# Performance work log

Hardware: AMD Instinct MI355X
Metric: run time of the kernel (lower is better)

## Reference

```python
import jax, jax.numpy as jnp
import numpy as np

NUM_HEADS = 16

def setup_inputs() -> dict:
    key = jax.random.key(0)
    ks = jax.random.split(key, 5)
    d_model = 1024
    x = jax.random.normal(ks[0], (2, 2048, d_model), dtype=jnp.float32)
    # xavier-uniform-like scale for square [d_model, d_model] weights
    lim = float(np.sqrt(6.0 / (d_model + d_model)))
    def w(k):
        return jax.random.uniform(k, (d_model, d_model), dtype=jnp.float32, minval=-lim, maxval=lim)
    return {"x": x, "Wq": w(ks[1]), "Wk": w(ks[2]), "Wv": w(ks[3]), "Wo": w(ks[4])}

def reference(x, Wq, Wk, Wv, Wo):
    B, S, D = x.shape
    H = NUM_HEADS
    dk = D // H
    # project: torch does x @ W.T
    def split_heads(t):
        return t.reshape(B, S, H, dk).transpose(0, 2, 1, 3)  # [B,H,S,dk]
    q = split_heads(x @ Wq.T)
    k = split_heads(x @ Wk.T)
    v = split_heads(x @ Wv.T)
    scores = jnp.einsum('bhqd,bhkd->bhqk', q, k) / jnp.sqrt(jnp.float32(dk))
    causal = jnp.tril(jnp.ones((S, S), dtype=bool))  # True where attended
    scores = jnp.where(causal[None, None], scores, -jnp.inf)
    probs = jax.nn.softmax(scores, axis=-1)
    out = jnp.einsum('bhqk,bhkd->bhqd', probs, v)  # [B,H,S,dk]
    out = out.transpose(0, 2, 1, 3).reshape(B, S, D)
    return out @ Wo.T
```

## Files before the change

### kernel.cpp

```cpp
#include <hip/hip_runtime.h>
#include <stdint.h>

#define BATCH  2
#define SEQ    2048
#define DMODEL 1024
#define NHEADS 16
#define DKH    64
#define MTOT   (BATCH*SEQ)
#define VSTR   (SEQ + 32)

typedef unsigned short u16;
typedef __bf16 bf16x8 __attribute__((ext_vector_type(8)));
typedef float  f32x4  __attribute__((ext_vector_type(4)));

extern "C" __device__ float __ocml_native_exp2_f32(float);

__device__ __forceinline__ u16 f2bf(float f) {
  union { float f; uint32_t u; } v; v.f = f;
  uint32_t u = v.u;
  return (u16)((u + 0x7FFFu + ((u >> 16) & 1u)) >> 16);
}
__device__ __forceinline__ float bf2f(u16 h) {
  union { uint32_t u; float f; } v; v.u = (uint32_t)h << 16; return v.f;
}

__device__ __forceinline__ void gld_lds16(const void* g, void* l) {
  __builtin_amdgcn_global_load_lds(
      (__attribute__((address_space(1))) void*)g,
      (__attribute__((address_space(3))) void*)l, 16, 0, 0);
}

__device__ __forceinline__ uint32_t cvtpk(float lo, float hi) {
  uint32_t r;
  asm("v_cvt_pk_bf16_f32 %0, %1, %2" : "=v"(r) : "v"(lo), "v"(hi));
  return r;
}
__device__ __forceinline__ void pl16swap(uint32_t& a, uint32_t& b) {
  asm volatile("v_permlane16_swap_b32 %0, %1" : "+v"(a), "+v"(b));
}

__global__ void cvt_all(const float* __restrict__ x, const float* __restrict__ wa,
                        const float* __restrict__ wb, const float* __restrict__ wc,
                        const float* __restrict__ wd,
                        u16* __restrict__ xb, u16* __restrict__ wdst) {
  const int blk = blockIdx.x;
  const int tid = threadIdx.x;
  if (blk < 4096) {
    size_t o = (size_t)blk * 1024 + tid * 4;
    float4 f = *(const float4*)(x + o);
    ushort4 p;
    p.x = f2bf(f.x); p.y = f2bf(f.y); p.z = f2bf(f.z); p.w = f2bf(f.w);
    *(ushort4*)(xb + o) = p;
  } else {
    int j = blk - 4096;
    const float* ws[4] = {wa, wb, wc, wd};
    size_t src_o = (size_t)(j & 1023) * 1024 + tid * 4;
    size_t dst_o = (size_t)j * 1024 + tid * 4;
    float4 f = *(const float4*)(ws[j >> 10] + src_o);
    ushort4 p;
    p.x = f2bf(f.x); p.y = f2bf(f.y); p.z = f2bf(f.z); p.w = f2bf(f.w);
    *(ushort4*)(wdst + dst_o) = p;
  }
}

__global__ __launch_bounds__(256, 3) void gemm_qkv(
    const u16* __restrict__ xb, const u16* __restrict__ wq,
    const u16* __restrict__ wk, const u16* __restrict__ wv,
    u16* __restrict__ q, u16* __restrict__ k, u16* __restrict__ v, float qscale) {
  __shared__ __align__(16) u16 lA[128 * 64];
  __shared__ __align__(16) u16 lB[3][64 * 64];

  const int tid  = threadIdx.x;
  const int lane = tid & 63;
  const int lrow = lane & 15;
  const int quad = lane >> 4;
  const int wave = tid >> 6;
  const int wm   = (wave & 1) * 64;
  const int wn   = (wave >> 1) * 32;
  const int sx   = lrow & 7;
  const int m0 = blockIdx.x * 128, n0 = blockIdx.y * 64;
  const u16* Ws[3] = {wq, wk, wv};

  f32x4 acc[3][4][2] = {};

  for (int k0 = 0; k0 < DMODEL; k0 += 64) {
    #pragma unroll
    for (int r = 0; r < 4; ++r) {
      int off  = r * 4096 + tid * 16;
      int row  = off >> 7;
      int c16  = (off >> 4) & 7;
      int colb = (c16 ^ (row & 7)) << 4;
      gld_lds16((const char*)xb + ((size_t)(m0 + row) * DMODEL + k0) * 2 + colb,
                (char*)lA + off);
    }
    #pragma unroll
    for (int z = 0; z < 3; ++z)
      #pragma unroll
      for (int r = 0; r < 2; ++r) {
        int off  = r * 4096 + tid * 16;
        int row  = off >> 7;
        int c16  = (off >> 4) & 7;
        int colb = (c16 ^ (row & 7)) << 4;
        gld_lds16((const char*)Ws[z] + ((size_t)(n0 + row) * DMODEL + k0) * 2 + colb,
                  (char*)&lB[z][0] + off);
      }
    __syncthreads();
    #pragma unroll
    for (int ks = 0; ks < 2; ++ks) {
      const int ro = ((((ks << 2) | quad) ^ sx) << 3);
      bf16x8 a[4], b[3][2];
      #pragma unroll
      for (int i = 0; i < 4; ++i)
        a[i] = *(const bf16x8*)(lA + (wm + i*16 + lrow) * 64 + ro);
      #pragma unroll
      for (int z = 0; z < 3; ++z)
        #pragma unroll
        for (int j = 0; j < 2; ++j)
          b[z][j] = *(const bf16x8*)(&lB[z][0] + (wn + j*16 + lrow) * 64 + ro);
      #pragma unroll
      for (int z = 0; z < 3; ++z)
        #pragma unroll
        for (int i = 0; i < 4; ++i)
          #pragma unroll
          for (int j = 0; j < 2; ++j)
            acc[z][i][j] = __builtin_amdgcn_mfma_f32_16x16x32_bf16(a[i], b[z][j], acc[z][i][j], 0, 0, 0);
    }
    __syncthreads();
  }

  const int rb = quad * 4, cb = lrow;
  const int h  = blockIdx.y;
  u16* outs[3] = {q, k, v};
  #pragma unroll
  for (int z = 0; z < 3; ++z) {
    u16* out = outs[z];
    if (z == 2) {
      #pragma unroll
      for (int i = 0; i < 4; ++i)
        #pragma unroll
        for (int j = 0; j < 2; ++j) {
          int row0 = m0 + wm + i*16 + rb;
          int d_   = wn + j*16 + cb;
          int b_ = row0 >> 11, s0 = row0 & 2047;
          ushort4 pk;
          pk.x = f2bf(acc[z][i][j][0]); pk.y = f2bf(acc[z][i][j][1]);
          pk.z = f2bf(acc[z][i][j][2]); pk.w = f2bf(acc[z][i][j][3]);
          *(ushort4*)&out[((size_t)(b_*NHEADS + h) * DKH + d_) * VSTR + s0] = pk;
        }
    } else {
      const float scale = (z == 0) ? qscale : 1.0f;
      #pragma unroll
      for (int i = 0; i < 4; ++i)
        #pragma unroll
        for (int j = 0; j < 2; ++j)
          #pragma unroll
          for (int r = 0; r < 4; ++r) {
            int row = m0 + wm + i*16 + rb + r;
            int d_  = wn + j*16 + cb;
            int b_ = row >> 11, s_ = row & 2047;
            out[(((size_t)(b_*NHEADS + h) * SEQ + s_) << 6) + d_] =
                f2bf(acc[z][i][j][r] * scale);
          }
    }
  }
}

__device__ __forceinline__ void gemm_core64(const u16* A, const u16* W,
                                            int m0, int n0, f32x4 acc[4][2],
                                            u16* lA, u16* lB) {
  const int tid  = threadIdx.x;
  const int lane = tid & 63;
  const int lrow = lane & 15;
  const int quad = lane >> 4;
  const int wave = tid >> 6;
  const int wm   = (wave & 1) * 64;
  const int wn   = (wave >> 1) * 32;
  const int sx   = lrow & 7;

  for (int k0 = 0; k0 < DMODEL; k0 += 64) {
    #pragma unroll
    for (int r = 0; r < 4; ++r) {
      int off  = r * 4096 + tid * 16;
      int row  = off >> 7;
      int c16  = (off >> 4) & 7;
      int colb = (c16 ^ (row & 7)) << 4;
      gld_lds16((const char*)A + ((size_t)(m0 + row) * DMODEL + k0) * 2 + colb,
                (char*)lA + off);
    }
    #pragma unroll
    for (int r = 0; r < 2; ++r) {
      int off  = r * 4096 + tid * 16;
      int row  = off >> 7;
      int c16  = (off >> 4) & 7;
      int colb = (c16 ^ (row & 7)) << 4;
      gld_lds16((const char*)W + ((size_t)(n0 + row) * DMODEL + k0) * 2 + colb,
                (char*)lB + off);
    }
    __syncthreads();
    #pragma unroll
    for (int ks = 0; ks < 2; ++ks) {
      bf16x8 a[4], b[2];
      const int ro = ((((ks << 2) | quad) ^ sx) << 3);
      #pragma unroll
      for (int i = 0; i < 4; ++i)
        a[i] = *(const bf16x8*)(lA + (wm + i*16 + lrow) * 64 + ro);
      #pragma unroll
      for (int j = 0; j < 2; ++j)
        b[j] = *(const bf16x8*)(lB + (wn + j*16 + lrow) * 64 + ro);
      #pragma unroll
      for (int i = 0; i < 4; ++i)
        #pragma unroll
        for (int j = 0; j < 2; ++j)
          acc[i][j] = __builtin_amdgcn_mfma_f32_16x16x32_bf16(a[i], b[j], acc[i][j], 0, 0, 0);
    }
    __syncthreads();
  }
}

__global__ __launch_bounds__(256, 3) void gemm_out(
    const u16* __restrict__ ab, const u16* __restrict__ wo, float* __restrict__ out) {
  __shared__ __align__(16) u16 lA[128 * 64];
  __shared__ __align__(16) u16 lB[64 * 64];
  const int m0 = blockIdx.x * 128, n0 = blockIdx.y * 64;
  f32x4 acc[4][2] = {};
  gemm_core64(ab, wo, m0, n0, acc, lA, lB);

  const int lane = threadIdx.x & 63;
  const int wave = threadIdx.x >> 6;
  const int wm = (wave & 1) * 64, wn = (wave >> 1) * 32;
  const int rb = (lane >> 4) * 4, cb = lane & 15;
  #pragma unroll
  for (int i = 0; i < 4; ++i)
    #pragma unroll
    for (int j = 0; j < 2; ++j)
      #pragma unroll
      for (int r = 0; r < 4; ++r)
        out[(size_t)(m0 + wm + i*16 + rb + r) * DMODEL + (n0 + wn + j*16 + cb)]
            = acc[i][j][r];
}

__device__ const uint8_t JT[40] = {
  60,61,62,63, 56,57,58, 52,53,54, 48,49,50, 44,45,46, 40,41, 36,37,
  32,33, 28,29, 24, 20, 16, 12,
  59,42,25,8, 55,38,21,4, 51,34,17,0
};

__device__ __forceinline__ void stage_kv(const u16* Kg, const u16* Vg, int t,
                                         u16* lK, u16* lV, int tid) {
  #pragma unroll
  for (int r = 0; r < 2; ++r) {
    int off  = r * 4096 + tid * 16;
    int row  = off >> 7;
    int colb = (((off >> 4) & 7) ^ (row & 7)) << 4;
    gld_lds16((const char*)Kg + ((size_t)(t*64 + row) * DKH) * 2 + colb,
              (char*)lK + off);
    gld_lds16((const char*)Vg + ((size_t)row * VSTR + t*64) * 2 + colb,
              (char*)lV + off);
  }
}

__global__ __launch_bounds__(256, 3) void attn(
    const u16* __restrict__ Q, const u16* __restrict__ K,
    const u16* __restrict__ V, u16* __restrict__ O,
    u16* __restrict__ po, float* __restrict__ pl) {
  __shared__ __align__(16) u16 lK[2][64 * 64];
  __shared__ __align__(16) u16 lV[2][64 * 64];

  const int tid  = threadIdx.x;
  const int wid  = tid >> 6;
  const int lane = tid & 63;
  const int lrow = lane & 15;
  const int quad = lane >> 4;
  const int sx   = lrow & 7;
  const int pq   = ((quad & 1) << 1) | (quad >> 1);

  const int g  = blockIdx.x >> 5;
  const int bh = blockIdx.x & 31;
  const int e  = JT[g];
  const int u  = e >> 2, c = e & 3;
  const int lo = c * 8;
  const int T  = 2*u + 2;
  const int hi = (lo + 8 < T) ? lo + 8 : T;
  const int td = 2*u + (wid >> 1);
  const int qg0 = 128*u + 32*wid;

  const u16* Qg = Q + (size_t)bh * SEQ * DKH;
  const u16* Kg = K + (size_t)bh * SEQ * DKH;
  const u16* Vg = V + (size_t)bh * DKH * VSTR;

  bf16x8 aq[2][2];
  #pragma unroll
  for (int i = 0; i < 2; ++i)
    #pragma unroll
    for (int ks = 0; ks < 2; ++ks)
      aq[i][ks] = *(const bf16x8*)(Qg + (size_t)(qg0 + 16*i + lrow) * DKH + ks*32 + quad*8);

  f32x4 o_acc[2][4] = {};
  float l_acc[2] = {};

  stage_kv(Kg, Vg, lo, &lK[0][0], &lV[0][0], tid);
  __syncthreads();
  int cur = 0;

  for (int t = lo; t < hi; ++t) {
    if (t + 1 < hi)
      stage_kv(Kg, Vg, t + 1, &lK[cur ^ 1][0], &lV[cur ^ 1][0], tid);

    if (t <= td) {
      f32x4 s_acc[2][4] = {};
      {
        bf16x8 kf[2][4];
        #pragma unroll
        for (int ks = 0; ks < 2; ++ks) {
          const int kro = ((((ks << 2) | quad) ^ sx) << 3);
          #pragma unroll
          for (int j = 0; j < 4; ++j)
            kf[ks][j] = *(const bf16x8*)(&lK[cur][0] + (j*16 + lrow) * 64 + kro);
        }
        __builtin_amdgcn_s_setprio(1);
        #pragma unroll
        for (int i = 0; i < 2; ++i)
          #pragma unroll
          for (int ks = 0; ks < 2; ++ks)
            #pragma unroll
            for (int j = 0; j < 4; ++j)
              s_acc[i][j] = __builtin_amdgcn_mfma_f32_16x16x32_bf16(kf[ks][j], aq[i][ks], s_acc[i][j], 0, 0, 0);
        __builtin_amdgcn_s_setprio(0);
      }

      bf16x8 vf[2][4];
      #pragma unroll
      for (int ks = 0; ks < 2; ++ks) {
        const int vro = ((((ks << 2) | pq) ^ sx) << 3);
        #pragma unroll
        for (int j = 0; j < 4; ++j)
          vf[ks][j] = *(const bf16x8*)(&lV[cur][0] + (j*16 + lrow) * 64 + vro);
      }

      #pragma unroll
      for (int i = 0; i < 2; ++i) {
        if (t >= td) {
          const int qrel = qg0 + 16*i + lrow - 64*t;
          #pragma unroll
          for (int j = 0; j < 4; ++j) {
            int kl = j*16 + quad*4;
            #pragma unroll
            for (int r = 0; r < 4; ++r)
              if (kl + r > qrel) s_acc[i][j][r] = -1e30f;
          }
        }

        uint32_t w[4][2];
        float ls = 0.f;
        #pragma unroll
        for (int j = 0; j < 4; ++j) {
          float p0 = __ocml_native_exp2_f32(s_acc[i][j][0]);
          float p1 = __ocml_native_exp2_f32(s_acc[i][j][1]);
          float p2 = __ocml_native_exp2_f32(s_acc[i][j][2]);
          float p3 = __ocml_native_exp2_f32(s_acc[i][j][3]);
          ls += (p0 + p1) + (p2 + p3);
          w[j][0] = cvtpk(p0, p1);
          w[j][1] = cvtpk(p2, p3);
        }
        l_acc[i] += ls;

        pl16swap(w[0][0], w[1][0]);
        pl16swap(w[0][1], w[1][1]);
        pl16swap(w[2][0], w[3][0]);
        pl16swap(w[2][1], w[3][1]);
        union { uint32_t u[4]; bf16x8 v; } g0, g1;
        g0.u[0] = w[0][0]; g0.u[1] = w[0][1]; g0.u[2] = w[1][0]; g0.u[3] = w[1][1];
        g1.u[0] = w[2][0]; g1.u[1] = w[2][1]; g1.u[2] = w[3][0]; g1.u[3] = w[3][1];

        __builtin_amdgcn_s_setprio(1);
        #pragma unroll
        for (int j = 0; j < 4; ++j)
          o_acc[i][j] = __builtin_amdgcn_mfma_f32_16x16x32_bf16(g0.v, vf[0][j], o_acc[i][j], 0, 0, 0);
        #pragma unroll
        for (int j = 0; j < 4; ++j)
          o_acc[i][j] = __builtin_amdgcn_mfma_f32_16x16x32_bf16(g1.v, vf[1][j], o_acc[i][j], 0, 0, 0);
        __builtin_amdgcn_s_setprio(0);
      }
    }

    __syncthreads();
    cur ^= 1;
  }

  float lr[2][4];
  #pragma unroll
  for (int i = 0; i < 2; ++i) {
    float s = l_acc[i];
    s += __shfl_xor(s, 16, 64);
    s += __shfl_xor(s, 32, 64);
    #pragma unroll
    for (int r = 0; r < 4; ++r)
      lr[i][r] = __shfl(s, quad*4 + r, 16);
  }

  if (T <= 8) {
    const int h = bh & 15, b_ = bh >> 4;
    #pragma unroll
    for (int i = 0; i < 2; ++i)
      #pragma unroll
      for (int j = 0; j < 4; ++j)
        #pragma unroll
        for (int r = 0; r < 4; ++r) {
          int sg = qg0 + 16*i + quad*4 + r;
          O[(size_t)(b_ * SEQ + sg) * DMODEL + h * DKH + j*16 + lrow]
              = f2bf(o_acc[i][j][r] / lr[i][r]);
        }
  } else {
    const int pold = td;
    const int base = (pold < 16) ? (pold - 8) * 2
                   : (pold < 24) ? 16 + (pold - 16) * 3
                   :               40 + (pold - 24) * 4;
    const int slot = (base + c) * 32 + bh;
    const int r64  = 32 * (wid & 1);
    #pragma unroll
    for (int i = 0; i < 2; ++i) {
      #pragma unroll
      for (int j = 0; j < 4; ++j) {
        ushort4 pk;
        pk.x = f2bf(o_acc[i][j][0]); pk.y = f2bf(o_acc[i][j][1]);
        pk.z = f2bf(o_acc[i][j][2]); pk.w = f2bf(o_acc[i][j][3]);
        *(ushort4*)&po[(size_t)slot * 4096 + (j*16 + lrow) * 64 + r64 + 16*i + quad*4] = pk;
      }
      if (lrow == 0)
        #pragma unroll
        for (int r = 0; r < 4; ++r)
          pl[slot * 64 + r64 + 16*i + quad*4 + r] = lr[i][r];
    }
  }
}

__global__ __launch_bounds__(256) void combine(
    const u16* __restrict__ po, const float* __restrict__ pl, u16* __restrict__ ab) {
  __shared__ u16 Ls[64][68];
  const int b  = blockIdx.x;
  const int p  = 8 + (b >> 5);
  const int bh = b & 31;
  const int t  = threadIdx.x;
  const int col = t >> 2;
  const int r0  = (t & 3) * 16;
  const int base = (p < 16) ? (p - 8) * 2
                 : (p < 24) ? 16 + (p - 16) * 3
                 :            40 + (p - 24) * 4;
  const int nc   = (p < 16) ? 2 : (p < 24) ? 3 : 4;

  float acc[16], lsum[16];
  const size_t s0 = (size_t)(base * 32 + bh);
  const u16*   q0 = po + s0 * 4096 + col * 64 + r0;
  const float* l0 = pl + s0 * 64 + r0;
  #pragma unroll
  for (int q4 = 0; q4 < 4; ++q4) {
    ushort4 a  = *(const ushort4*)(q0 + q4 * 4);
    ushort4 c2 = *(const ushort4*)(q0 + (size_t)32 * 4096 + q4 * 4);
    acc[q4*4+0] = bf2f(a.x) + bf2f(c2.x);
    acc[q4*4+1] = bf2f(a.y) + bf2f(c2.y);
    acc[q4*4+2] = bf2f(a.z) + bf2f(c2.z);
    acc[q4*4+3] = bf2f(a.w) + bf2f(c2.w);
    float4 f = *(const float4*)(l0 + q4 * 4);
    float4 g = *(const float4*)(l0 + 32 * 64 + q4 * 4);
    lsum[q4*4+0] = f.x + g.x; lsum[q4*4+1] = f.y + g.y;
    lsum[q4*4+2] = f.z + g.z; lsum[q4*4+3] = f.w + g.w;
  }
  if (nc >= 3) {
    #pragma unroll
    for (int q4 = 0; q4 < 4; ++q4) {
      ushort4 a = *(const ushort4*)(q0 + (size_t)64 * 4096 + q4 * 4);
      acc[q4*4+0] += bf2f(a.x); acc[q4*4+1] += bf2f(a.y);
      acc[q4*4+2] += bf2f(a.z); acc[q4*4+3] += bf2f(a.w);
      float4 f = *(const float4*)(l0 + 64 * 64 + q4 * 4);
      lsum[q4*4+0] += f.x; lsum[q4*4+1] += f.y;
      lsum[q4*4+2] += f.z; lsum[q4*4+3] += f.w;
    }
  }
  if (nc == 4) {
    #pragma unroll
    for (int q4 = 0; q4 < 4; ++q4) {
      ushort4 a = *(const ushort4*)(q0 + (size_t)96 * 4096 + q4 * 4);
      acc[q4*4+0] += bf2f(a.x); acc[q4*4+1] += bf2f(a.y);
      acc[q4*4+2] += bf2f(a.z); acc[q4*4+3] += bf2f(a.w);
      float4 f = *(const float4*)(l0 + 96 * 64 + q4 * 4);
      lsum[q4*4+0] += f.x; lsum[q4*4+1] += f.y;
      lsum[q4*4+2] += f.z; lsum[q4*4+3] += f.w;
    }
  }
  #pragma unroll
  for (int q = 0; q < 16; ++q)
    Ls[r0 + q][col] = f2bf(acc[q] / lsum[q]);
  __syncthreads();

  const int row = t >> 2;
  const int c0  = (t & 3) * 16;
  const int b_ = bh >> 4, h = bh & 15;
  u16* dst = ab + (size_t)(b_ * SEQ + 64 * p + row) * DMODEL + h * DKH + c0;
  #pragma unroll
  for (int q = 0; q < 16; q += 4)
    *(ushort4*)(dst + q) = *(const ushort4*)&Ls[row][c0 + q];
}

extern "C" void kernel_launch(void* const* d_in, const int* in_sizes, int n_in,
                              void* d_out, int out_size, void* d_ws, size_t ws_size,
                              hipStream_t stream) {
  const float* x  = (const float*)d_in[0];
  const float* Wq = (const float*)d_in[1];
  const float* Wk = (const float*)d_in[2];
  const float* Wv = (const float*)d_in[3];
  const float* Wo = (const float*)d_in[4];
  float* out = (float*)d_out;

  u16* xb  = (u16*)d_ws;
  u16* wqb = xb  + (size_t)MTOT * DMODEL;
  u16* wkb = wqb + (size_t)DMODEL * DMODEL;
  u16* wvb = wkb + (size_t)DMODEL * DMODEL;
  u16* wob = wvb + (size_t)DMODEL * DMODEL;
  u16* qb  = wob + (size_t)DMODEL * DMODEL;
  u16* kb  = qb  + (size_t)MTOT * DMODEL;
  u16* vb  = kb  + (size_t)MTOT * DMODEL;
  u16* ab  = vb  + (size_t)BATCH * NHEADS * DKH * VSTR;
  u16* po  = ab  + (size_t)MTOT * DMODEL;
  float* pl = (float*)(po + (size_t)2304 * 4096);

  cvt_all<<<8192, 256, 0, stream>>>(x, Wq, Wk, Wv, Wo, xb, wqb);

  const float qscale = 0.125f * 1.44269504088896340736f;
  gemm_qkv<<<dim3(32, 16), 256, 0, stream>>>(
      xb, wqb, wkb, wvb, qb, kb, vb, qscale);

  attn<<<1280, 256, 0, stream>>>(qb, kb, vb, ab, po, pl);
  combine<<<768, 256, 0, stream>>>(po, pl, ab);

  gemm_out<<<dim3(32, 16), 256, 0, stream>>>(ab, wob, out);
}
```

Before: 161.2 us.

## Double-buffer LDS tiles in QKV and output projection GEMMs

Both projection GEMMs now use two LDS buffers per operand. The next K-slice is loaded asynchronously while MFMA runs on the current one, and one barrier per iteration replaces two. This aims to hide global-to-LDS load latency behind compute. In exchange, LDS use doubles: QKV needs about 80KB per block, so its launch bound drops from 3 to 2 blocks per CU, and the output GEMM needs about 48KB per block.

```diff
diff --git a/kernel.cpp b/kernel.cpp
--- a/kernel.cpp
+++ b/kernel.cpp
@@ -63,12 +63,37 @@
   }
 }
 
-__global__ __launch_bounds__(256, 3) void gemm_qkv(
+__device__ __forceinline__ void stage_qkv(const u16* xb, const u16* w0,
+                                          const u16* w1, const u16* w2,
+                                          int m0, int n0, int k0, int tid,
+                                          u16* lA, u16* lB0) {
+  #pragma unroll
+  for (int r = 0; r < 4; ++r) {
+    int off  = r * 4096 + tid * 16;
+    int row  = off >> 7;
+    int colb = (((off >> 4) & 7) ^ (row & 7)) << 4;
+    gld_lds16((const char*)xb + ((size_t)(m0 + row) * DMODEL + k0) * 2 + colb,
+              (char*)lA + off);
+  }
+  const u16* Ws[3] = {w0, w1, w2};
+  #pragma unroll
+  for (int z = 0; z < 3; ++z)
+    #pragma unroll
+    for (int r = 0; r < 2; ++r) {
+      int off  = r * 4096 + tid * 16;
+      int row  = off >> 7;
+      int colb = (((off >> 4) & 7) ^ (row & 7)) << 4;
+      gld_lds16((const char*)Ws[z] + ((size_t)(n0 + row) * DMODEL + k0) * 2 + colb,
+                (char*)(lB0 + z * 4096) + off);
+    }
+}
+
+__global__ __launch_bounds__(256, 2) void gemm_qkv(
     const u16* __restrict__ xb, const u16* __restrict__ wq,
     const u16* __restrict__ wk, const u16* __restrict__ wv,
     u16* __restrict__ q, u16* __restrict__ k, u16* __restrict__ v, float qscale) {
-  __shared__ __align__(16) u16 lA[128 * 64];
-  __shared__ __align__(16) u16 lB[3][64 * 64];
+  __shared__ __align__(16) u16 lA[2][128 * 64];
+  __shared__ __align__(16) u16 lB[2][3][64 * 64];
 
   const int tid  = threadIdx.x;
   const int lane = tid & 63;
@@ -79,44 +104,29 @@
   const int wn   = (wave >> 1) * 32;
   const int sx   = lrow & 7;
   const int m0 = blockIdx.x * 128, n0 = blockIdx.y * 64;
-  const u16* Ws[3] = {wq, wk, wv};
 
   f32x4 acc[3][4][2] = {};
 
+  stage_qkv(xb, wq, wk, wv, m0, n0, 0, tid, &lA[0][0], &lB[0][0][0]);
+  __syncthreads();
+  int cur = 0;
+
   for (int k0 = 0; k0 < DMODEL; k0 += 64) {
-    #pragma unroll
-    for (int r = 0; r < 4; ++r) {
-      int off  = r * 4096 + tid * 16;
-      int row  = off >> 7;
-      int c16  = (off >> 4) & 7;
-      int colb = (c16 ^ (row & 7)) << 4;
-      gld_lds16((const char*)xb + ((size_t)(m0 + row) * DMODEL + k0) * 2 + colb,
-                (char*)lA + off);
-    }
-    #pragma unroll
-    for (int z = 0; z < 3; ++z)
-      #pragma unroll
-      for (int r = 0; r < 2; ++r) {
-        int off  = r * 4096 + tid * 16;
-        int row  = off >> 7;
-        int c16  = (off >> 4) & 7;
-        int colb = (c16 ^ (row & 7)) << 4;
-        gld_lds16((const char*)Ws[z] + ((size_t)(n0 + row) * DMODEL + k0) * 2 + colb,
-                  (char*)&lB[z][0] + off);
-      }
-    __syncthreads();
+    if (k0 + 64 < DMODEL)
+      stage_qkv(xb, wq, wk, wv, m0, n0, k0 + 64, tid,
+                &lA[cur ^ 1][0], &lB[cur ^ 1][0][0]);
     #pragma unroll
     for (int ks = 0; ks < 2; ++ks) {
       const int ro = ((((ks << 2) | quad) ^ sx) << 3);
       bf16x8 a[4], b[3][2];
       #pragma unroll
       for (int i = 0; i < 4; ++i)
-        a[i] = *(const bf16x8*)(lA + (wm + i*16 + lrow) * 64 + ro);
+        a[i] = *(const bf16x8*)(&lA[cur][0] + (wm + i*16 + lrow) * 64 + ro);
       #pragma unroll
       for (int z = 0; z < 3; ++z)
         #pragma unroll
         for (int j = 0; j < 2; ++j)
-          b[z][j] = *(const bf16x8*)(&lB[z][0] + (wn + j*16 + lrow) * 64 + ro);
+          b[z][j] = *(const bf16x8*)(&lB[cur][z][0] + (wn + j*16 + lrow) * 64 + ro);
       #pragma unroll
       for (int z = 0; z < 3; ++z)
         #pragma unroll
@@ -126,6 +136,7 @@
             acc[z][i][j] = __builtin_amdgcn_mfma_f32_16x16x32_bf16(a[i], b[z][j], acc[z][i][j], 0, 0, 0);
     }
     __syncthreads();
+    cur ^= 1;
   }
 
   const int rb = quad * 4, cb = lrow;
@@ -165,9 +176,33 @@
   }
 }
 
-__device__ __forceinline__ void gemm_core64(const u16* A, const u16* W,
-                                            int m0, int n0, f32x4 acc[4][2],
-                                            u16* lA, u16* lB) {
+__device__ __forceinline__ void stage_ab(const u16* A, const u16* W,
+                                         int m0, int n0, int k0, int tid,
+                                         u16* lA, u16* lB) {
+  #pragma unroll
+  for (int r = 0; r < 4; ++r) {
+    int off  = r * 4096 + tid * 16;
+    int row  = off >> 7;
+    int colb = (((off >> 4) & 7) ^ (row & 7)) << 4;
+    gld_lds16((const char*)A + ((size_t)(m0 + row) * DMODEL + k0) * 2 + colb,
+              (char*)lA + off);
+  }
+  #pragma unroll
+  for (int r = 0; r < 2; ++r) {
+    int off  = r * 4096 + tid * 16;
+    int row  = off >> 7;
+    int colb = (((off >> 4) & 7) ^ (row & 7)) << 4;
+    gld_lds16((const char*)W + ((size_t)(n0 + row) * DMODEL + k0) * 2 + colb,
+              (char*)lB + off);
+  }
+}
+
+__global__ __launch_bounds__(256, 3) void gemm_out(
+    const u16* __restrict__ ab, const u16* __restrict__ wo, float* __restrict__ out) {
+  __shared__ __align__(16) u16 lA[2][128 * 64];
+  __shared__ __align__(16) u16 lB[2][64 * 64];
+  const int m0 = blockIdx.x * 128, n0 = blockIdx.y * 64;
+
   const int tid  = threadIdx.x;
   const int lane = tid & 63;
   const int lrow = lane & 15;
@@ -177,36 +212,25 @@
   const int wn   = (wave >> 1) * 32;
   const int sx   = lrow & 7;
 
+  f32x4 acc[4][2] = {};
+
+  stage_ab(ab, wo, m0, n0, 0, tid, &lA[0][0], &lB[0][0]);
+  __syncthreads();
+  int cur = 0;
+
   for (int k0 = 0; k0 < DMODEL; k0 += 64) {
-    #pragma unroll
-    for (int r = 0; r < 4; ++r) {
-      int off  = r * 4096 + tid * 16;
-      int row  = off >> 7;
-      int c16  = (off >> 4) & 7;
-      int colb = (c16 ^ (row & 7)) << 4;
-      gld_lds16((const char*)A + ((size_t)(m0 + row) * DMODEL + k0) * 2 + colb,
-                (char*)lA + off);
-    }
-    #pragma unroll
-    for (int r = 0; r < 2; ++r) {
-      int off  = r * 4096 + tid * 16;
-      int row  = off >> 7;
-      int c16  = (off >> 4) & 7;
-      int colb = (c16 ^ (row & 7)) << 4;
-      gld_lds16((const char*)W + ((size_t)(n0 + row) * DMODEL + k0) * 2 + colb,
-                (char*)lB + off);
-    }
-    __syncthreads();
+    if (k0 + 64 < DMODEL)
+      stage_ab(ab, wo, m0, n0, k0 + 64, tid, &lA[cur ^ 1][0], &lB[cur ^ 1][0]);
     #pragma unroll
     for (int ks = 0; ks < 2; ++ks) {
       bf16x8 a[4], b[2];
       const int ro = ((((ks << 2) | quad) ^ sx) << 3);
       #pragma unroll
       for (int i = 0; i < 4; ++i)
-        a[i] = *(const bf16x8*)(lA + (wm + i*16 + lrow) * 64 + ro);
+        a[i] = *(const bf16x8*)(&lA[cur][0] + (wm + i*16 + lrow) * 64 + ro);
       #pragma unroll
       for (int j = 0; j < 2; ++j)
-        b[j] = *(const bf16x8*)(lB + (wn + j*16 + lrow) * 64 + ro);
+        b[j] = *(const bf16x8*)(&lB[cur][0] + (wn + j*16 + lrow) * 64 + ro);
       #pragma unroll
       for (int i = 0; i < 4; ++i)
         #pragma unroll
@@ -214,20 +238,9 @@
           acc[i][j] = __builtin_amdgcn_mfma_f32_16x16x32_bf16(a[i], b[j], acc[i][j], 0, 0, 0);
     }
     __syncthreads();
-  }
-}
-
-__global__ __launch_bounds__(256, 3) void gemm_out(
-    const u16* __restrict__ ab, const u16* __restrict__ wo, float* __restrict__ out) {
-  __shared__ __align__(16) u16 lA[128 * 64];
-  __shared__ __align__(16) u16 lB[64 * 64];
-  const int m0 = blockIdx.x * 128, n0 = blockIdx.y * 64;
-  f32x4 acc[4][2] = {};
-  gemm_core64(ab, wo, m0, n0, acc, lA, lB);
-
-  const int lane = threadIdx.x & 63;
-  const int wave = threadIdx.x >> 6;
-  const int wm = (wave & 1) * 64, wn = (wave >> 1) * 32;
+    cur ^= 1;
+  }
+
   const int rb = (lane >> 4) * 4, cb = lane & 15;
   #pragma unroll
   for (int i = 0; i < 4; ++i)
```

Measured after the change: 163.4 us. No clear change (+1.4%).
